# Kernel tuning notes

Hardware: AMD Instinct MI355X
Metric: run time of the kernel (lower is better)

Reference implementation:

```python
import jax, jax.numpy as jnp
import numpy as np

N_ITER = 5
NMF_EPS = 1e-20
IP_EPS = 1e-20

M, J, I, K = 2, 2000, 2049, 8  # channels == sources, frames, freq bins, NMF bases


def setup_inputs() -> dict:
    key = jax.random.key(0)
    k1, k2, k3 = jax.random.split(key, 3)
    X = jax.random.normal(k1, (M, J, I, 2), dtype=jnp.float32)
    lo = 1e-08
    T0 = jax.random.uniform(k2, (I, K, M), dtype=jnp.float32) * (1 - lo) + lo
    V0 = jax.random.uniform(k3, (K, J, M), dtype=jnp.float32) * (1 - lo) + lo
    return {"X": X, "T0": T0, "V0": V0}


def nmf_update(T, V, Y, eps):
    # T: (I,K), V: (K,J), Y: (I,J) complex
    P = jnp.abs(Y) ** 2                       # power spectrogram (I,J)
    R = T @ V                                  # low-rank model (I,J)
    T = T * jnp.sqrt(((P / (R * R)) @ V.T) / ((1.0 / R) @ V.T))
    T = jnp.maximum(T, eps)
    R = T @ V
    V = V * jnp.sqrt((T.T @ (P / (R * R))) / (T.T @ (1.0 / R)))
    V = jnp.maximum(V, eps)
    R = T @ V
    return T, V, R


def reference(X, T0, V0):
    Mc, Jc, Ic, _ = X.shape
    N = Mc
    # view_as_complex(X.permute(2,0,1,3)) -> (I, M, J) complex
    Xc = jnp.transpose(X[..., 0] + 1j * X[..., 1], (2, 0, 1)).astype(jnp.complex64)
    eye_M = jnp.eye(Mc, dtype=jnp.complex64)
    W = jnp.broadcast_to(eye_M, (Ic, N, Mc))   # (I, N, M)
    T, V = T0, V0

    def body(carry, _):
        W, T, V = carry
        Y = jnp.einsum('inm,imj->inj', W, Xc)  # (I, N, J)
        for n in range(N):
            Tn, Vn, Rn = nmf_update(T[:, :, n], V[:, :, n], Y[:, n, :], NMF_EPS)
            T = T.at[:, :, n].set(Tn)
            V = V.at[:, :, n].set(Vn)
            inv_Rn = 1.0 / (Rn + IP_EPS)                       # (I, J)
            Xw = Xc * jnp.sqrt(inv_Rn)[:, None, :]             # (I, M, J)
            D = jnp.einsum('imj,ikj->imk', Xw, jnp.conj(Xw)) / Jc  # (I, M, M)
            Dreg = D + IP_EPS * eye_M
            A = jnp.einsum('inm,imk->ink', W, Dreg)            # (I, M, M)
            e_n = jnp.broadcast_to(eye_M[:, n], (Ic, Mc))
            b = jnp.linalg.solve(A, e_n[..., None])[..., 0]    # (I, M)
            quad = jnp.einsum('im,imk,ik->i', jnp.conj(b), Dreg, b)
            denom = jnp.sqrt(jnp.real(quad) + IP_EPS)          # (I,)
            W = W.at[:, n, :].set(jnp.conj(b / denom[:, None]))
        return (W, T, V), None

    (W, T, V), _ = jax.lax.scan(body, (W, T, V), None, length=N_ITER)
    Y = jnp.einsum('inm,imj->inj', W, Xc)                      # (I, N, J)
    Yp = jnp.transpose(Y, (1, 2, 0))                           # (N, J, I)
    return jnp.stack([jnp.real(Yp), jnp.imag(Yp)], axis=-1)    # (N, J, I, 2)
```

## Files before the change

### kernel.cpp

```cpp
#include <hip/hip_runtime.h>
#include <hip/hip_bf16.h>

#define M_CH 2
#define J_F 2000
#define I_F 2049
#define K_B 8
#define N_IT 5
#define NMF_EPS 1e-20f
#define IP_EPS 1e-20f

__global__ void k_init(const float* __restrict__ T0, const float* __restrict__ V0,
                       float* __restrict__ T, float* __restrict__ V, float* __restrict__ W) {
  int t = blockIdx.x * blockDim.x + threadIdx.x;
  int stride = gridDim.x * blockDim.x;
  for (int idx = t; idx < 2 * I_F * K_B; idx += stride) {
    int n = idx / (I_F * K_B);
    int r = idx % (I_F * K_B);
    int i = r / K_B, k = r % K_B;
    T[idx] = T0[(i * K_B + k) * M_CH + n];
  }
  for (int idx = t; idx < 2 * K_B * J_F; idx += stride) {
    int n = idx / (K_B * J_F);
    int r = idx % (K_B * J_F);
    int k = r / J_F, j = r % J_F;
    V[idx] = V0[(k * J_F + j) * M_CH + n];
  }
  for (int i = t; i < I_F; i += stride) {
    W[i * 8 + 0] = 1.f; W[i * 8 + 1] = 0.f; W[i * 8 + 2] = 0.f; W[i * 8 + 3] = 0.f;
    W[i * 8 + 4] = 0.f; W[i * 8 + 5] = 0.f; W[i * 8 + 6] = 1.f; W[i * 8 + 7] = 0.f;
  }
}

__global__ __launch_bounds__(256) void k_pack(const float2* __restrict__ X,
                                              float4* __restrict__ Xp) {
  const int i = blockIdx.x * 256 + threadIdx.x;
  if (i >= I_F) return;
  const int j0 = blockIdx.y * 8;
  const int jend = min(8, J_F - j0);
  for (int jj = 0; jj < jend; ++jj) {
    const int j = j0 + jj;
    float2 a = X[(size_t)j * I_F + i];
    float2 b = X[(size_t)(J_F + j) * I_F + i];
    Xp[(size_t)j * I_F + i] = make_float4(a.x, a.y, b.x, b.y);
  }
}

__global__ __launch_bounds__(256) void k_packT(const float2* __restrict__ X,
                                               float4* __restrict__ Xpt) {
  __shared__ float4 Tl[32][33];
  const int tid = threadIdx.x;
  const int i0 = blockIdx.x * 32, j0 = blockIdx.y * 32;
  const int la = tid & 31, su = tid >> 5;
#pragma unroll
  for (int p = 0; p < 4; ++p) {
    int jj = su + p * 8;
    int i = i0 + la, j = j0 + jj;
    if (i < I_F && j < J_F) {
      float2 a = X[(size_t)j * I_F + i];
      float2 b = X[(size_t)(J_F + j) * I_F + i];
      Tl[la][jj] = make_float4(a.x, a.y, b.x, b.y);
    }
  }
  __syncthreads();
#pragma unroll
  for (int p = 0; p < 4; ++p) {
    int ii = su + p * 8;
    int i = i0 + ii, j = j0 + la;
    if (i < I_F && j < J_F) Xpt[(size_t)i * J_F + j] = Tl[ii][la];
  }
}

__device__ __forceinline__ float4 load_x(const float4* Xp, const float2* X,
                                         int pk, size_t j, int i) {
  if (pk) return Xp[j * I_F + i];
  float2 a = X[j * I_F + i];
  float2 b = X[(size_t)J_F * I_F + j * I_F + i];
  return make_float4(a.x, a.y, b.x, b.y);
}

__device__ __forceinline__ float4 load_xt(const float4* Xpt, const float2* X,
                                          int pk, int i, int j) {
  if (pk) return Xpt[(size_t)i * J_F + j];
  float2 a = X[(size_t)j * I_F + i];
  float2 b = X[(size_t)(J_F + j) * I_F + i];
  return make_float4(a.x, a.y, b.x, b.y);
}

template<int PK>
__global__ __launch_bounds__(256) void k_T_rows(const float4* __restrict__ Xpt,
                                                const float2* __restrict__ X,
                                                const float* __restrict__ W,
                                                float* __restrict__ T,
                                                const float* __restrict__ V) {
  const int i = blockIdx.x;
  const int tid = threadIdx.x;
  float tr0[K_B], tr1[K_B];
#pragma unroll
  for (int k = 0; k < K_B; ++k) {
    tr0[k] = T[(size_t)i * 8 + k];
    tr1[k] = T[((size_t)I_F + i) * 8 + k];
  }
  const float4 w0 = ((const float4*)W)[i * 2];
  const float4 w1 = ((const float4*)W)[i * 2 + 1];
  float num0[K_B] = {}, den0[K_B] = {}, num1[K_B] = {}, den1[K_B] = {};
  for (int j = tid; j < J_F; j += 256) {
    float4 x = load_xt(Xpt, X, PK, i, j);
    float yr = w0.x * x.x - w0.y * x.y + w0.z * x.z - w0.w * x.w;
    float yi = w0.x * x.y + w0.y * x.x + w0.z * x.w + w0.w * x.z;
    float p0 = yr * yr + yi * yi;
    float zr = w1.x * x.x - w1.y * x.y + w1.z * x.z - w1.w * x.w;
    float zi = w1.x * x.y + w1.y * x.x + w1.z * x.w + w1.w * x.z;
    float p1 = zr * zr + zi * zi;
    float v0[K_B], v1[K_B];
    float R0 = 0.f, R1 = 0.f;
#pragma unroll
    for (int k = 0; k < K_B; ++k) {
      v0[k] = V[(size_t)k * J_F + j];           R0 += tr0[k] * v0[k];
      v1[k] = V[(size_t)(K_B + k) * J_F + j];   R1 += tr1[k] * v1[k];
    }
    float a0 = p0 / (R0 * R0), b0 = 1.0f / R0;
    float a1 = p1 / (R1 * R1), b1 = 1.0f / R1;
#pragma unroll
    for (int k = 0; k < K_B; ++k) {
      num0[k] += a0 * v0[k]; den0[k] += b0 * v0[k];
      num1[k] += a1 * v1[k]; den1[k] += b1 * v1[k];
    }
  }
  __shared__ float red[4][32];
  const int lane = tid & 63, wid = tid >> 6;
#pragma unroll
  for (int k = 0; k < K_B; ++k) {
    float a0 = num0[k], b0 = den0[k], a1 = num1[k], b1 = den1[k];
#pragma unroll
    for (int off = 32; off > 0; off >>= 1) {
      a0 += __shfl_xor(a0, off, 64);
      b0 += __shfl_xor(b0, off, 64);
      a1 += __shfl_xor(a1, off, 64);
      b1 += __shfl_xor(b1, off, 64);
    }
    if (lane == 0) {
      red[wid][k] = a0; red[wid][8 + k] = b0;
      red[wid][16 + k] = a1; red[wid][24 + k] = b1;
    }
  }
  __syncthreads();
  if (tid < 32) red[0][tid] = red[0][tid] + red[1][tid] + red[2][tid] + red[3][tid];
  __syncthreads();
  if (tid < 16) {
    int n = tid >> 3, k = tid & 7;
    float nu = red[0][n * 16 + k];
    float de = red[0][n * 16 + 8 + k];
    size_t idx = ((size_t)n * I_F + i) * 8 + k;
    float told = T[idx];
    T[idx] = fmaxf(told * sqrtf(nu / de), NMF_EPS);
  }
}

template<int PK>
__global__ __launch_bounds__(256) void k_v_update(const float4* __restrict__ Xp,
                                                  const float2* __restrict__ X,
                                                  const float* __restrict__ W,
                                                  const float* __restrict__ T,
                                                  float* __restrict__ V) {
  const int j = blockIdx.x;
  const int tid = threadIdx.x;
  float vold0[K_B], vold1[K_B];
#pragma unroll
  for (int k = 0; k < K_B; ++k) {
    vold0[k] = V[(size_t)k * J_F + j];
    vold1[k] = V[(size_t)(K_B + k) * J_F + j];
  }
  float num0[K_B] = {}, den0[K_B] = {}, num1[K_B] = {}, den1[K_B] = {};
  const float* T1 = T + (size_t)I_F * K_B;
  for (int i = tid; i < I_F; i += 256) {
    float4 x = load_x(Xp, X, PK, (size_t)j, i);
    const float4 wa = ((const float4*)W)[i * 2];
    const float4 wb = ((const float4*)W)[i * 2 + 1];
    float yr = wa.x * x.x - wa.y * x.y + wa.z * x.z - wa.w * x.w;
    float yi = wa.x * x.y + wa.y * x.x + wa.z * x.w + wa.w * x.z;
    float p0 = yr * yr + yi * yi;
    float zr = wb.x * x.x - wb.y * x.y + wb.z * x.z - wb.w * x.w;
    float zi = wb.x * x.y + wb.y * x.x + wb.z * x.w + wb.w * x.z;
    float p1 = zr * zr + zi * zi;
    const float4 ta = *(const float4*)&T[i * 8];
    const float4 tb = *(const float4*)&T[i * 8 + 4];
    const float4 tc = *(const float4*)&T1[i * 8];
    const float4 td = *(const float4*)&T1[i * 8 + 4];
    float t0[K_B] = {ta.x, ta.y, ta.z, ta.w, tb.x, tb.y, tb.z, tb.w};
    float t1[K_B] = {tc.x, tc.y, tc.z, tc.w, td.x, td.y, td.z, td.w};
    float R0 = 0.f, R1 = 0.f;
#pragma unroll
    for (int k = 0; k < K_B; ++k) { R0 += t0[k] * vold0[k]; R1 += t1[k] * vold1[k]; }
    float a0 = p0 / (R0 * R0), b0 = 1.0f / R0;
    float a1 = p1 / (R1 * R1), b1 = 1.0f / R1;
#pragma unroll
    for (int k = 0; k < K_B; ++k) {
      num0[k] += a0 * t0[k]; den0[k] += b0 * t0[k];
      num1[k] += a1 * t1[k]; den1[k] += b1 * t1[k];
    }
  }
  __shared__ float red[4][32];
  const int lane = tid & 63, wid = tid >> 6;
#pragma unroll
  for (int k = 0; k < K_B; ++k) {
    float a0 = num0[k], b0 = den0[k], a1 = num1[k], b1 = den1[k];
#pragma unroll
    for (int off = 32; off > 0; off >>= 1) {
      a0 += __shfl_xor(a0, off, 64);
      b0 += __shfl_xor(b0, off, 64);
      a1 += __shfl_xor(a1, off, 64);
      b1 += __shfl_xor(b1, off, 64);
    }
    if (lane == 0) {
      red[wid][k] = a0; red[wid][8 + k] = b0;
      red[wid][16 + k] = a1; red[wid][24 + k] = b1;
    }
  }
  __syncthreads();
  if (tid < 32) red[0][tid] = red[0][tid] + red[1][tid] + red[2][tid] + red[3][tid];
  __syncthreads();
  if (tid < 16) {
    int n = tid >> 3, k = tid & 7;
    float nu = red[0][n * 16 + k];
    float de = red[0][n * 16 + 8 + k];
    size_t idx = ((size_t)n * K_B + k) * J_F + j;
    float vo = V[idx];
    V[idx] = fmaxf(vo * sqrtf(nu / de), NMF_EPS);
  }
}

template<int PK>
__global__ __launch_bounds__(256) void k_d_rows(const float4* __restrict__ Xpt,
                                                const float2* __restrict__ X,
                                                const float* __restrict__ T,
                                                const float* __restrict__ V,
                                                float* __restrict__ W) {
  const int i = blockIdx.x;
  const int tid = threadIdx.x;
  float tr0[K_B], tr1[K_B];
#pragma unroll
  for (int k = 0; k < K_B; ++k) {
    tr0[k] = T[(size_t)i * K_B + k];
    tr1[k] = T[((size_t)I_F + i) * K_B + k];
  }
  float acc[8] = {};
  for (int j = tid; j < J_F; j += 256) {
    float4 x = load_xt(Xpt, X, PK, i, j);
    float R0 = 0.f, R1 = 0.f;
#pragma unroll
    for (int k = 0; k < K_B; ++k) {
      R0 += tr0[k] * V[(size_t)k * J_F + j];
      R1 += tr1[k] * V[(size_t)(K_B + k) * J_F + j];
    }
    float wv0 = 1.0f / (R0 + IP_EPS);
    float wv1 = 1.0f / (R1 + IP_EPS);
    float p00 = x.x * x.x + x.y * x.y;
    float p11 = x.z * x.z + x.w * x.w;
    float pr = x.x * x.z + x.y * x.w;
    float pi = x.y * x.z - x.x * x.w;
    acc[0] += wv0 * p00; acc[1] += wv0 * p11; acc[2] += wv0 * pr; acc[3] += wv0 * pi;
    acc[4] += wv1 * p00; acc[5] += wv1 * p11; acc[6] += wv1 * pr; acc[7] += wv1 * pi;
  }
  __shared__ float red[4][8];
  const int lane = tid & 63, wid = tid >> 6;
#pragma unroll
  for (int v = 0; v < 8; ++v) {
    float a = acc[v];
#pragma unroll
    for (int off = 32; off > 0; off >>= 1) a += __shfl_xor(a, off, 64);
    if (lane == 0) red[wid][v] = a;
  }
  __syncthreads();
  if (tid < 8) red[0][tid] = red[0][tid] + red[1][tid] + red[2][tid] + red[3][tid];
  __syncthreads();
  if (tid == 0) {
    float4 wa = ((const float4*)W)[i * 2];
    float4 wb = ((const float4*)W)[i * 2 + 1];
    float w00r = wa.x, w00i = wa.y, w01r = wa.z, w01i = wa.w;
    float w10r = wb.x, w10i = wb.y, w11r = wb.z, w11i = wb.w;
    const float invJ = 1.0f / (float)J_F;
#pragma unroll
    for (int n = 0; n < 2; ++n) {
      float d00 = red[0][n * 4 + 0] * invJ + IP_EPS;
      float d11 = red[0][n * 4 + 1] * invJ + IP_EPS;
      float d01r = red[0][n * 4 + 2] * invJ;
      float d01i = red[0][n * 4 + 3] * invJ;
      float A00r = w00r * d00 + (w01r * d01r + w01i * d01i);
      float A00i = w00i * d00 + (w01i * d01r - w01r * d01i);
      float A01r = (w00r * d01r - w00i * d01i) + w01r * d11;
      float A01i = (w00r * d01i + w00i * d01r) + w01i * d11;
      float A10r = w10r * d00 + (w11r * d01r + w11i * d01i);
      float A10i = w10i * d00 + (w11i * d01r - w11r * d01i);
      float A11r = (w10r * d01r - w10i * d01i) + w11r * d11;
      float A11i = (w10r * d01i + w10i * d01r) + w11i * d11;
      float detr = (A00r * A11r - A00i * A11i) - (A01r * A10r - A01i * A10i);
      float deti = (A00r * A11i + A00i * A11r) - (A01r * A10i + A01i * A10r);
      float idet = 1.0f / (detr * detr + deti * deti);
      float n0r, n0i, n1r, n1i;
      if (n == 0) { n0r = A11r; n0i = A11i; n1r = -A10r; n1i = -A10i; }
      else        { n0r = -A01r; n0i = -A01i; n1r = A00r; n1i = A00i; }
      float b0r = (n0r * detr + n0i * deti) * idet;
      float b0i = (n0i * detr - n0r * deti) * idet;
      float b1r = (n1r * detr + n1i * deti) * idet;
      float b1i = (n1i * detr - n1r * deti) * idet;
      float cr = d01r * b1r - d01i * b1i;
      float ci = d01r * b1i + d01i * b1r;
      float quad = d00 * (b0r * b0r + b0i * b0i) + d11 * (b1r * b1r + b1i * b1i)
                 + 2.0f * (b0r * cr + b0i * ci);
      float s = 1.0f / sqrtf(quad + IP_EPS);
      if (n == 0) { w00r = b0r * s; w00i = -b0i * s; w01r = b1r * s; w01i = -b1i * s; }
      else        { w10r = b0r * s; w10i = -b0i * s; w11r = b1r * s; w11i = -b1i * s; }
    }
    ((float4*)W)[i * 2]     = make_float4(w00r, w00i, w01r, w01i);
    ((float4*)W)[i * 2 + 1] = make_float4(w10r, w10i, w11r, w11i);
  }
}

template<int PK>
__global__ __launch_bounds__(256) void k_final(const float4* __restrict__ Xp,
                                               const float2* __restrict__ X,
                                               const float* __restrict__ W,
                                               float2* __restrict__ out) {
  const int i = blockIdx.x * 256 + threadIdx.x;
  if (i >= I_F) return;
  const float4 wa = ((const float4*)W)[i * 2];
  const float4 wb = ((const float4*)W)[i * 2 + 1];
  const int j0 = blockIdx.y * 8;
  const int jend = min(8, J_F - j0);
  for (int jj = 0; jj < jend; ++jj) {
    const int j = j0 + jj;
    float4 x = load_x(Xp, X, PK, (size_t)j, i);
    float y0r = wa.x * x.x - wa.y * x.y + wa.z * x.z - wa.w * x.w;
    float y0i = wa.x * x.y + wa.y * x.x + wa.z * x.w + wa.w * x.z;
    out[(size_t)j * I_F + i] = make_float2(y0r, y0i);
    float y1r = wb.x * x.x - wb.y * x.y + wb.z * x.z - wb.w * x.w;
    float y1i = wb.x * x.y + wb.y * x.x + wb.z * x.w + wb.w * x.z;
    out[(size_t)(J_F + j) * I_F + i] = make_float2(y1r, y1i);
  }
}

extern "C" void kernel_launch(void* const* d_in, const int* in_sizes, int n_in,
                              void* d_out, int out_size, void* d_ws, size_t ws_size,
                              hipStream_t stream) {
  const float2* X = (const float2*)d_in[0];
  const float* T0 = (const float*)d_in[1];
  const float* V0 = (const float*)d_in[2];
  char* ws = (char*)d_ws;
  size_t off = 0;
  auto alloc = [&](size_t bytes) -> void* {
    void* p = ws + off;
    off = (off + bytes + 255) & ~(size_t)255;
    return p;
  };
  float* W = (float*)alloc((size_t)I_F * 8 * 4);
  float* T = (float*)alloc((size_t)2 * I_F * K_B * 4);
  float* V = (float*)alloc((size_t)2 * K_B * J_F * 4);
  const size_t x_sz = (size_t)J_F * I_F * 16;
  float4* Xpt = nullptr;
  float4* Xp = nullptr;
  if (off + x_sz <= ws_size) Xpt = (float4*)alloc(x_sz);
  if (Xpt && off + x_sz <= ws_size) Xp = (float4*)alloc(x_sz);
  const int pkt = Xpt != nullptr, pkj = Xp != nullptr;

  k_init<<<128, 256, 0, stream>>>(T0, V0, T, V, W);
  if (pkt) k_packT<<<dim3(65, 63), 256, 0, stream>>>(X, Xpt);
  if (pkj) k_pack<<<dim3(9, 250), 256, 0, stream>>>(X, Xp);

  if (pkt && pkj) {
    for (int it = 0; it < N_IT; ++it) {
      k_T_rows<1><<<I_F, 256, 0, stream>>>(Xpt, X, W, T, V);
      k_v_update<1><<<J_F, 256, 0, stream>>>(Xp, X, W, T, V);
      k_d_rows<1><<<I_F, 256, 0, stream>>>(Xpt, X, T, V, W);
    }
    k_final<1><<<dim3(9, 250), 256, 0, stream>>>(Xp, X, W, (float2*)d_out);
  } else if (pkt) {
    for (int it = 0; it < N_IT; ++it) {
      k_T_rows<1><<<I_F, 256, 0, stream>>>(Xpt, X, W, T, V);
      k_v_update<0><<<J_F, 256, 0, stream>>>(nullptr, X, W, T, V);
      k_d_rows<1><<<I_F, 256, 0, stream>>>(Xpt, X, T, V, W);
    }
    k_final<0><<<dim3(9, 250), 256, 0, stream>>>(nullptr, X, W, (float2*)d_out);
  } else {
    for (int it = 0; it < N_IT; ++it) {
      k_T_rows<0><<<I_F, 256, 0, stream>>>(nullptr, X, W, T, V);
      k_v_update<0><<<J_F, 256, 0, stream>>>(nullptr, X, W, T, V);
      k_d_rows<0><<<I_F, 256, 0, stream>>>(nullptr, X, T, V, W);
    }
    k_final<0><<<dim3(9, 250), 256, 0, stream>>>(nullptr, X, W, (float2*)d_out);
  }
}
```

Measured before the change: 490.2 us.

## Store packed X copies in fp16, fuse setup kernels, process two frames per thread

The two packed copies of X (row-major and transposed) are now stored as half precision instead of float4, which halves the bytes streamed by the T, V and D kernels in every iteration. The init, pack and transpose-pack kernels are merged into one setup launch. The T and D kernels now handle two frames per thread with 16-byte loads. The final output kernel reads the original fp32 X. Storing X in fp16 loses precision in the power and covariance terms, which could push results past the accuracy tolerance.

After: 467.9 us. 1.05x faster.

```diff
diff --git a/kernel.cpp b/kernel.cpp
--- a/kernel.cpp
+++ b/kernel.cpp
@@ -1,5 +1,5 @@
 #include <hip/hip_runtime.h>
-#include <hip/hip_bf16.h>
+#include <hip/hip_fp16.h>
 
 #define M_CH 2
 #define J_F 2000
@@ -9,10 +9,81 @@
 #define NMF_EPS 1e-20f
 #define IP_EPS 1e-20f
 
-__global__ void k_init(const float* __restrict__ T0, const float* __restrict__ V0,
-                       float* __restrict__ T, float* __restrict__ V, float* __restrict__ W) {
-  int t = blockIdx.x * blockDim.x + threadIdx.x;
-  int stride = gridDim.x * blockDim.x;
+#define NB_PACKT (65 * 63)
+#define NB_PACK (9 * 250)
+#define NB_INIT 128
+
+__device__ __forceinline__ float2 h2f(unsigned u) {
+  __half2 h = *reinterpret_cast<__half2*>(&u);
+  return __half22float2(h);
+}
+__device__ __forceinline__ float4 h4f(unsigned lo, unsigned hi) {
+  float2 a = h2f(lo), b = h2f(hi);
+  return make_float4(a.x, a.y, b.x, b.y);
+}
+__device__ __forceinline__ unsigned f2h(float a, float b) {
+  __half2 h = __floats2half2_rn(a, b);
+  return *reinterpret_cast<unsigned*>(&h);
+}
+
+template<int PK>
+__global__ __launch_bounds__(256) void k_setup(const float2* __restrict__ X,
+                                               const float* __restrict__ T0,
+                                               const float* __restrict__ V0,
+                                               float* __restrict__ T,
+                                               float* __restrict__ V,
+                                               float* __restrict__ W,
+                                               __half* __restrict__ Xht,
+                                               __half* __restrict__ Xhj) {
+  int b = blockIdx.x;
+  const int tid = threadIdx.x;
+  if (b < NB_PACKT) {
+    if (!PK) return;
+    __shared__ float4 Tl[32][33];
+    const int i0 = (b % 65) * 32, j0 = (b / 65) * 32;
+    const int la = tid & 31, su = tid >> 5;
+#pragma unroll
+    for (int p = 0; p < 4; ++p) {
+      int jj = su + p * 8;
+      int i = i0 + la, j = j0 + jj;
+      if (i < I_F && j < J_F) {
+        float2 a = X[(size_t)j * I_F + i];
+        float2 c = X[(size_t)(J_F + j) * I_F + i];
+        Tl[la][jj] = make_float4(a.x, a.y, c.x, c.y);
+      }
+    }
+    __syncthreads();
+#pragma unroll
+    for (int p = 0; p < 4; ++p) {
+      int ii = su + p * 8;
+      int i = i0 + ii, j = j0 + la;
+      if (i < I_F && j < J_F) {
+        float4 x = Tl[ii][la];
+        *(uint2*)(Xht + ((size_t)i * J_F + j) * 4) =
+            make_uint2(f2h(x.x, x.y), f2h(x.z, x.w));
+      }
+    }
+    return;
+  }
+  b -= NB_PACKT;
+  if (b < NB_PACK) {
+    if (!PK) return;
+    const int i = (b % 9) * 256 + tid;
+    if (i >= I_F) return;
+    const int j0 = (b / 9) * 8;
+    const int jend = min(8, J_F - j0);
+    for (int jj = 0; jj < jend; ++jj) {
+      const int j = j0 + jj;
+      float2 a = X[(size_t)j * I_F + i];
+      float2 c = X[(size_t)(J_F + j) * I_F + i];
+      *(uint2*)(Xhj + ((size_t)j * I_F + i) * 4) =
+          make_uint2(f2h(a.x, a.y), f2h(c.x, c.y));
+    }
+    return;
+  }
+  b -= NB_PACK;
+  int t = b * 256 + tid;
+  const int stride = NB_INIT * 256;
   for (int idx = t; idx < 2 * I_F * K_B; idx += stride) {
     int n = idx / (I_F * K_B);
     int r = idx % (I_F * K_B);
@@ -31,67 +102,12 @@
   }
 }
 
-__global__ __launch_bounds__(256) void k_pack(const float2* __restrict__ X,
-                                              float4* __restrict__ Xp) {
-  const int i = blockIdx.x * 256 + threadIdx.x;
-  if (i >= I_F) return;
-  const int j0 = blockIdx.y * 8;
-  const int jend = min(8, J_F - j0);
-  for (int jj = 0; jj < jend; ++jj) {
-    const int j = j0 + jj;
-    float2 a = X[(size_t)j * I_F + i];
-    float2 b = X[(size_t)(J_F + j) * I_F + i];
-    Xp[(size_t)j * I_F + i] = make_float4(a.x, a.y, b.x, b.y);
-  }
-}
-
-__global__ __launch_bounds__(256) void k_packT(const float2* __restrict__ X,
-                                               float4* __restrict__ Xpt) {
-  __shared__ float4 Tl[32][33];
-  const int tid = threadIdx.x;
-  const int i0 = blockIdx.x * 32, j0 = blockIdx.y * 32;
-  const int la = tid & 31, su = tid >> 5;
-#pragma unroll
-  for (int p = 0; p < 4; ++p) {
-    int jj = su + p * 8;
-    int i = i0 + la, j = j0 + jj;
-    if (i < I_F && j < J_F) {
-      float2 a = X[(size_t)j * I_F + i];
-      float2 b = X[(size_t)(J_F + j) * I_F + i];
-      Tl[la][jj] = make_float4(a.x, a.y, b.x, b.y);
-    }
-  }
-  __syncthreads();
-#pragma unroll
-  for (int p = 0; p < 4; ++p) {
-    int ii = su + p * 8;
-    int i = i0 + ii, j = j0 + la;
-    if (i < I_F && j < J_F) Xpt[(size_t)i * J_F + j] = Tl[ii][la];
-  }
-}
-
-__device__ __forceinline__ float4 load_x(const float4* Xp, const float2* X,
-                                         int pk, size_t j, int i) {
-  if (pk) return Xp[j * I_F + i];
-  float2 a = X[j * I_F + i];
-  float2 b = X[(size_t)J_F * I_F + j * I_F + i];
-  return make_float4(a.x, a.y, b.x, b.y);
-}
-
-__device__ __forceinline__ float4 load_xt(const float4* Xpt, const float2* X,
-                                          int pk, int i, int j) {
-  if (pk) return Xpt[(size_t)i * J_F + j];
-  float2 a = X[(size_t)j * I_F + i];
-  float2 b = X[(size_t)(J_F + j) * I_F + i];
-  return make_float4(a.x, a.y, b.x, b.y);
-}
-
 template<int PK>
-__global__ __launch_bounds__(256) void k_T_rows(const float4* __restrict__ Xpt,
-                                                const float2* __restrict__ X,
-                                                const float* __restrict__ W,
-                                                float* __restrict__ T,
-                                                const float* __restrict__ V) {
+__global__ __launch_bounds__(256) void k_T(const __half* __restrict__ Xht,
+                                           const float2* __restrict__ X,
+                                           const float* __restrict__ W,
+                                           float* __restrict__ T,
+                                           const float* __restrict__ V) {
   const int i = blockIdx.x;
   const int tid = threadIdx.x;
   float tr0[K_B], tr1[K_B];
@@ -103,27 +119,72 @@
   const float4 w0 = ((const float4*)W)[i * 2];
   const float4 w1 = ((const float4*)W)[i * 2 + 1];
   float num0[K_B] = {}, den0[K_B] = {}, num1[K_B] = {}, den1[K_B] = {};
-  for (int j = tid; j < J_F; j += 256) {
-    float4 x = load_xt(Xpt, X, PK, i, j);
-    float yr = w0.x * x.x - w0.y * x.y + w0.z * x.z - w0.w * x.w;
-    float yi = w0.x * x.y + w0.y * x.x + w0.z * x.w + w0.w * x.z;
-    float p0 = yr * yr + yi * yi;
-    float zr = w1.x * x.x - w1.y * x.y + w1.z * x.z - w1.w * x.w;
-    float zi = w1.x * x.y + w1.y * x.x + w1.z * x.w + w1.w * x.z;
-    float p1 = zr * zr + zi * zi;
-    float v0[K_B], v1[K_B];
-    float R0 = 0.f, R1 = 0.f;
-#pragma unroll
-    for (int k = 0; k < K_B; ++k) {
-      v0[k] = V[(size_t)k * J_F + j];           R0 += tr0[k] * v0[k];
-      v1[k] = V[(size_t)(K_B + k) * J_F + j];   R1 += tr1[k] * v1[k];
-    }
-    float a0 = p0 / (R0 * R0), b0 = 1.0f / R0;
-    float a1 = p1 / (R1 * R1), b1 = 1.0f / R1;
-#pragma unroll
-    for (int k = 0; k < K_B; ++k) {
-      num0[k] += a0 * v0[k]; den0[k] += b0 * v0[k];
-      num1[k] += a1 * v1[k]; den1[k] += b1 * v1[k];
+  if (PK) {
+    const __half* xrow = Xht + (size_t)i * J_F * 4;
+    for (int j2 = tid; j2 < J_F / 2; j2 += 256) {
+      const int j = j2 * 2;
+      uint4 raw = *(const uint4*)(xrow + (size_t)j * 4);
+      float4 xa = h4f(raw.x, raw.y);
+      float4 xb = h4f(raw.z, raw.w);
+      float2 v0p[K_B], v1p[K_B];
+      float R0a = 0.f, R0b = 0.f, R1a = 0.f, R1b = 0.f;
+#pragma unroll
+      for (int k = 0; k < K_B; ++k) {
+        v0p[k] = *(const float2*)&V[(size_t)k * J_F + j];
+        v1p[k] = *(const float2*)&V[(size_t)(K_B + k) * J_F + j];
+        R0a += tr0[k] * v0p[k].x; R0b += tr0[k] * v0p[k].y;
+        R1a += tr1[k] * v1p[k].x; R1b += tr1[k] * v1p[k].y;
+      }
+      float yr, yi;
+      yr = w0.x * xa.x - w0.y * xa.y + w0.z * xa.z - w0.w * xa.w;
+      yi = w0.x * xa.y + w0.y * xa.x + w0.z * xa.w + w0.w * xa.z;
+      float p0a = yr * yr + yi * yi;
+      yr = w1.x * xa.x - w1.y * xa.y + w1.z * xa.z - w1.w * xa.w;
+      yi = w1.x * xa.y + w1.y * xa.x + w1.z * xa.w + w1.w * xa.z;
+      float p1a = yr * yr + yi * yi;
+      yr = w0.x * xb.x - w0.y * xb.y + w0.z * xb.z - w0.w * xb.w;
+      yi = w0.x * xb.y + w0.y * xb.x + w0.z * xb.w + w0.w * xb.z;
+      float p0b = yr * yr + yi * yi;
+      yr = w1.x * xb.x - w1.y * xb.y + w1.z * xb.z - w1.w * xb.w;
+      yi = w1.x * xb.y + w1.y * xb.x + w1.z * xb.w + w1.w * xb.z;
+      float p1b = yr * yr + yi * yi;
+      float a0a = p0a / (R0a * R0a), b0a = 1.f / R0a;
+      float a1a = p1a / (R1a * R1a), b1a = 1.f / R1a;
+      float a0b = p0b / (R0b * R0b), b0b = 1.f / R0b;
+      float a1b = p1b / (R1b * R1b), b1b = 1.f / R1b;
+#pragma unroll
+      for (int k = 0; k < K_B; ++k) {
+        num0[k] += a0a * v0p[k].x + a0b * v0p[k].y;
+        den0[k] += b0a * v0p[k].x + b0b * v0p[k].y;
+        num1[k] += a1a * v1p[k].x + a1b * v1p[k].y;
+        den1[k] += b1a * v1p[k].x + b1b * v1p[k].y;
+      }
+    }
+  } else {
+    for (int j = tid; j < J_F; j += 256) {
+      float2 a = X[(size_t)j * I_F + i];
+      float2 c = X[(size_t)(J_F + j) * I_F + i];
+      float4 x = make_float4(a.x, a.y, c.x, c.y);
+      float yr = w0.x * x.x - w0.y * x.y + w0.z * x.z - w0.w * x.w;
+      float yi = w0.x * x.y + w0.y * x.x + w0.z * x.w + w0.w * x.z;
+      float p0 = yr * yr + yi * yi;
+      float zr = w1.x * x.x - w1.y * x.y + w1.z * x.z - w1.w * x.w;
+      float zi = w1.x * x.y + w1.y * x.x + w1.z * x.w + w1.w * x.z;
+      float p1 = zr * zr + zi * zi;
+      float v0[K_B], v1[K_B];
+      float R0 = 0.f, R1 = 0.f;
+#pragma unroll
+      for (int k = 0; k < K_B; ++k) {
+        v0[k] = V[(size_t)k * J_F + j];         R0 += tr0[k] * v0[k];
+        v1[k] = V[(size_t)(K_B + k) * J_F + j]; R1 += tr1[k] * v1[k];
+      }
+      float a0 = p0 / (R0 * R0), b0 = 1.0f / R0;
+      float a1 = p1 / (R1 * R1), b1 = 1.0f / R1;
+#pragma unroll
+      for (int k = 0; k < K_B; ++k) {
+        num0[k] += a0 * v0[k]; den0[k] += b0 * v0[k];
+        num1[k] += a1 * v1[k]; den1[k] += b1 * v1[k];
+      }
     }
   }
   __shared__ float red[4][32];
@@ -157,11 +218,11 @@
 }
 
 template<int PK>
-__global__ __launch_bounds__(256) void k_v_update(const float4* __restrict__ Xp,
-                                                  const float2* __restrict__ X,
-                                                  const float* __restrict__ W,
-                                                  const float* __restrict__ T,
-                                                  float* __restrict__ V) {
+__global__ __launch_bounds__(256) void k_V(const __half* __restrict__ Xhj,
+                                           const float2* __restrict__ X,
+                                           const float* __restrict__ W,
+                                           const float* __restrict__ T,
+                                           float* __restrict__ V) {
   const int j = blockIdx.x;
   const int tid = threadIdx.x;
   float vold0[K_B], vold1[K_B];
@@ -172,8 +233,17 @@
   }
   float num0[K_B] = {}, den0[K_B] = {}, num1[K_B] = {}, den1[K_B] = {};
   const float* T1 = T + (size_t)I_F * K_B;
+  const __half* xcol = Xhj + (size_t)j * I_F * 4;
   for (int i = tid; i < I_F; i += 256) {
-    float4 x = load_x(Xp, X, PK, (size_t)j, i);
+    float4 x;
+    if (PK) {
+      uint2 raw = *(const uint2*)(xcol + (size_t)i * 4);
+      x = h4f(raw.x, raw.y);
+    } else {
+      float2 a = X[(size_t)j * I_F + i];
+      float2 c = X[(size_t)(J_F + j) * I_F + i];
+      x = make_float4(a.x, a.y, c.x, c.y);
+    }
     const float4 wa = ((const float4*)W)[i * 2];
     const float4 wb = ((const float4*)W)[i * 2 + 1];
     float yr = wa.x * x.x - wa.y * x.y + wa.z * x.z - wa.w * x.w;
@@ -230,11 +300,11 @@
 }
 
 template<int PK>
-__global__ __launch_bounds__(256) void k_d_rows(const float4* __restrict__ Xpt,
-                                                const float2* __restrict__ X,
-                                                const float* __restrict__ T,
-                                                const float* __restrict__ V,
-                                                float* __restrict__ W) {
+__global__ __launch_bounds__(256) void k_D(const __half* __restrict__ Xht,
+                                           const float2* __restrict__ X,
+                                           const float* __restrict__ T,
+                                           const float* __restrict__ V,
+                                           float* __restrict__ W) {
   const int i = blockIdx.x;
   const int tid = threadIdx.x;
   float tr0[K_B], tr1[K_B];
@@ -244,22 +314,56 @@
     tr1[k] = T[((size_t)I_F + i) * K_B + k];
   }
   float acc[8] = {};
-  for (int j = tid; j < J_F; j += 256) {
-    float4 x = load_xt(Xpt, X, PK, i, j);
-    float R0 = 0.f, R1 = 0.f;
-#pragma unroll
-    for (int k = 0; k < K_B; ++k) {
-      R0 += tr0[k] * V[(size_t)k * J_F + j];
-      R1 += tr1[k] * V[(size_t)(K_B + k) * J_F + j];
-    }
-    float wv0 = 1.0f / (R0 + IP_EPS);
-    float wv1 = 1.0f / (R1 + IP_EPS);
-    float p00 = x.x * x.x + x.y * x.y;
-    float p11 = x.z * x.z + x.w * x.w;
-    float pr = x.x * x.z + x.y * x.w;
-    float pi = x.y * x.z - x.x * x.w;
-    acc[0] += wv0 * p00; acc[1] += wv0 * p11; acc[2] += wv0 * pr; acc[3] += wv0 * pi;
-    acc[4] += wv1 * p00; acc[5] += wv1 * p11; acc[6] += wv1 * pr; acc[7] += wv1 * pi;
+  if (PK) {
+    const __half* xrow = Xht + (size_t)i * J_F * 4;
+    for (int j2 = tid; j2 < J_F / 2; j2 += 256) {
+      const int j = j2 * 2;
+      uint4 raw = *(const uint4*)(xrow + (size_t)j * 4);
+      float4 xa = h4f(raw.x, raw.y);
+      float4 xb = h4f(raw.z, raw.w);
+      float R0a = 0.f, R0b = 0.f, R1a = 0.f, R1b = 0.f;
+#pragma unroll
+      for (int k = 0; k < K_B; ++k) {
+        float2 v0p = *(const float2*)&V[(size_t)k * J_F + j];
+        float2 v1p = *(const float2*)&V[(size_t)(K_B + k) * J_F + j];
+        R0a += tr0[k] * v0p.x; R0b += tr0[k] * v0p.y;
+        R1a += tr1[k] * v1p.x; R1b += tr1[k] * v1p.y;
+      }
+      float wv0a = 1.0f / (R0a + IP_EPS), wv0b = 1.0f / (R0b + IP_EPS);
+      float wv1a = 1.0f / (R1a + IP_EPS), wv1b = 1.0f / (R1b + IP_EPS);
+      float p00a = xa.x * xa.x + xa.y * xa.y, p00b = xb.x * xb.x + xb.y * xb.y;
+      float p11a = xa.z * xa.z + xa.w * xa.w, p11b = xb.z * xb.z + xb.w * xb.w;
+      float pra = xa.x * xa.z + xa.y * xa.w, prb = xb.x * xb.z + xb.y * xb.w;
+      float pia = xa.y * xa.z - xa.x * xa.w, pib = xb.y * xb.z - xb.x * xb.w;
+      acc[0] += wv0a * p00a + wv0b * p00b;
+      acc[1] += wv0a * p11a + wv0b * p11b;
+      acc[2] += wv0a * pra + wv0b * prb;
+      acc[3] += wv0a * pia + wv0b * pib;
+      acc[4] += wv1a * p00a + wv1b * p00b;
+      acc[5] += wv1a * p11a + wv1b * p11b;
+      acc[6] += wv1a * pra + wv1b * prb;
+      acc[7] += wv1a * pia + wv1b * pib;
+    }
+  } else {
+    for (int j = tid; j < J_F; j += 256) {
+      float2 a = X[(size_t)j * I_F + i];
+      float2 c = X[(size_t)(J_F + j) * I_F + i];
+      float4 x = make_float4(a.x, a.y, c.x, c.y);
+      float R0 = 0.f, R1 = 0.f;
+#pragma unroll
+      for (int k = 0; k < K_B; ++k) {
+        R0 += tr0[k] * V[(size_t)k * J_F + j];
+        R1 += tr1[k] * V[(size_t)(K_B + k) * J_F + j];
+      }
+      float wv0 = 1.0f / (R0 + IP_EPS);
+      float wv1 = 1.0f / (R1 + IP_EPS);
+      float p00 = x.x * x.x + x.y * x.y;
+      float p11 = x.z * x.z + x.w * x.w;
+      float pr = x.x * x.z + x.y * x.w;
+      float pi = x.y * x.z - x.x * x.w;
+      acc[0] += wv0 * p00; acc[1] += wv0 * p11; acc[2] += wv0 * pr; acc[3] += wv0 * pi;
+      acc[4] += wv1 * p00; acc[5] += wv1 * p11; acc[6] += wv1 * pr; acc[7] += wv1 * pi;
+    }
   }
   __shared__ float red[4][8];
   const int lane = tid & 63, wid = tid >> 6;
@@ -316,9 +420,7 @@
   }
 }
 
-template<int PK>
-__global__ __launch_bounds__(256) void k_final(const float4* __restrict__ Xp,
-                                               const float2* __restrict__ X,
+__global__ __launch_bounds__(256) void k_final(const float2* __restrict__ X,
                                                const float* __restrict__ W,
                                                float2* __restrict__ out) {
   const int i = blockIdx.x * 256 + threadIdx.x;
@@ -329,12 +431,13 @@
   const int jend = min(8, J_F - j0);
   for (int jj = 0; jj < jend; ++jj) {
     const int j = j0 + jj;
-    float4 x = load_x(Xp, X, PK, (size_t)j, i);
-    float y0r = wa.x * x.x - wa.y * x.y + wa.z * x.z - wa.w * x.w;
-    float y0i = wa.x * x.y + wa.y * x.x + wa.z * x.w + wa.w * x.z;
+    float2 a = X[(size_t)j * I_F + i];
+    float2 c = X[(size_t)(J_F + j) * I_F + i];
+    float y0r = wa.x * a.x - wa.y * a.y + wa.z * c.x - wa.w * c.y;
+    float y0i = wa.x * a.y + wa.y * a.x + wa.z * c.y + wa.w * c.x;
     out[(size_t)j * I_F + i] = make_float2(y0r, y0i);
-    float y1r = wb.x * x.x - wb.y * x.y + wb.z * x.z - wb.w * x.w;
-    float y1i = wb.x * x.y + wb.y * x.x + wb.z * x.w + wb.w * x.z;
+    float y1r = wb.x * a.x - wb.y * a.y + wb.z * c.x - wb.w * c.y;
+    float y1i = wb.x * a.y + wb.y * a.x + wb.z * c.y + wb.w * c.x;
     out[(size_t)(J_F + j) * I_F + i] = make_float2(y1r, y1i);
   }
 }
@@ -345,6 +448,7 @@
   const float2* X = (const float2*)d_in[0];
   const float* T0 = (const float*)d_in[1];
   const float* V0 = (const float*)d_in[2];
+  float2* outp = (float2*)d_out;
   char* ws = (char*)d_ws;
   size_t off = 0;
   auto alloc = [&](size_t bytes) -> void* {
@@ -355,37 +459,29 @@
   float* W = (float*)alloc((size_t)I_F * 8 * 4);
   float* T = (float*)alloc((size_t)2 * I_F * K_B * 4);
   float* V = (float*)alloc((size_t)2 * K_B * J_F * 4);
-  const size_t x_sz = (size_t)J_F * I_F * 16;
-  float4* Xpt = nullptr;
-  float4* Xp = nullptr;
-  if (off + x_sz <= ws_size) Xpt = (float4*)alloc(x_sz);
-  if (Xpt && off + x_sz <= ws_size) Xp = (float4*)alloc(x_sz);
-  const int pkt = Xpt != nullptr, pkj = Xp != nullptr;
-
-  k_init<<<128, 256, 0, stream>>>(T0, V0, T, V, W);
-  if (pkt) k_packT<<<dim3(65, 63), 256, 0, stream>>>(X, Xpt);
-  if (pkj) k_pack<<<dim3(9, 250), 256, 0, stream>>>(X, Xp);
-
-  if (pkt && pkj) {
+  const size_t xh_sz = (size_t)J_F * I_F * 8;
+  __half* Xht = nullptr;
+  __half* Xhj = nullptr;
+  if (off + 2 * xh_sz + 512 <= ws_size) {
+    Xht = (__half*)alloc(xh_sz);
+    Xhj = (__half*)alloc(xh_sz);
+  }
+  const int NBS = NB_PACKT + NB_PACK + NB_INIT;
+
+  if (Xht) {
+    k_setup<1><<<NBS, 256, 0, stream>>>(X, T0, V0, T, V, W, Xht, Xhj);
     for (int it = 0; it < N_IT; ++it) {
-      k_T_rows<1><<<I_F, 256, 0, stream>>>(Xpt, X, W, T, V);
-      k_v_update<1><<<J_F, 256, 0, stream>>>(Xp, X, W, T, V);
-      k_d_rows<1><<<I_F, 256, 0, stream>>>(Xpt, X, T, V, W);
-    }
-    k_final<1><<<dim3(9, 250), 256, 0, stream>>>(Xp, X, W, (float2*)d_out);
-  } else if (pkt) {
+      k_T<1><<<I_F, 256, 0, stream>>>(Xht, X, W, T, V);
+      k_V<1><<<J_F, 256, 0, stream>>>(Xhj, X, W, T, V);
+      k_D<1><<<I_F, 256, 0, stream>>>(Xht, X, T, V, W);
+    }
+  } else {
+    k_setup<0><<<NBS, 256, 0, stream>>>(X, T0, V0, T, V, W, nullptr, nullptr);
     for (int it = 0; it < N_IT; ++it) {
-      k_T_rows<1><<<I_F, 256, 0, stream>>>(Xpt, X, W, T, V);
-      k_v_update<0><<<J_F, 256, 0, stream>>>(nullptr, X, W, T, V);
-      k_d_rows<1><<<I_F, 256, 0, stream>>>(Xpt, X, T, V, W);
-    }
-    k_final<0><<<dim3(9, 250), 256, 0, stream>>>(nullptr, X, W, (float2*)d_out);
-  } else {
-    for (int it = 0; it < N_IT; ++it) {
-      k_T_rows<0><<<I_F, 256, 0, stream>>>(nullptr, X, W, T, V);
-      k_v_update<0><<<J_F, 256, 0, stream>>>(nullptr, X, W, T, V);
-      k_d_rows<0><<<I_F, 256, 0, stream>>>(nullptr, X, T, V, W);
-    }
-    k_final<0><<<dim3(9, 250), 256, 0, stream>>>(nullptr, X, W, (float2*)d_out);
-  }
-}
+      k_T<0><<<I_F, 256, 0, stream>>>(nullptr, X, W, T, V);
+      k_V<0><<<J_F, 256, 0, stream>>>(nullptr, X, W, T, V);
+      k_D<0><<<I_F, 256, 0, stream>>>(nullptr, X, T, V, W);
+    }
+  }
+  k_final<<<dim3(9, 250), 256, 0, stream>>>(X, W, outp);
+}
```
